# Performance work log

Hardware: AMD Instinct MI355X
Metric: run time of the kernel (lower is better)

## Reference

```python
import jax, jax.numpy as jnp
import numpy as np

N_NODES = 50000
N_EDGES = 800000
N_GRAPHS = 64
IN_CH = 128
HID_G = 256
HID_FC = 256
OUT_CH = 128


def setup_inputs() -> dict:
    key = jax.random.key(0)
    ks = jax.random.split(key, 16)
    x = jax.random.normal(ks[0], (N_NODES, IN_CH), dtype=jnp.float32)
    edge_index = jax.random.randint(ks[1], (2, N_EDGES), 0, N_NODES, dtype=jnp.int64)
    batch = jnp.sort(jax.random.randint(ks[2], (N_NODES,), 0, N_GRAPHS, dtype=jnp.int64))
    hlr = jax.random.normal(ks[3], (N_GRAPHS, 1), dtype=jnp.float32)
    std = jax.random.normal(ks[4], (N_GRAPHS, 1), dtype=jnp.float32)
    s = 0.05
    W0 = jax.random.normal(ks[5], (IN_CH, HID_G), dtype=jnp.float32) * s
    b0 = jnp.zeros((HID_G,), jnp.float32)
    W1 = jax.random.normal(ks[6], (HID_G, HID_G), dtype=jnp.float32) * s
    b1 = jnp.zeros((HID_G,), jnp.float32)
    W2 = jax.random.normal(ks[7], (HID_G, HID_G), dtype=jnp.float32) * s
    b2 = jnp.zeros((HID_G,), jnp.float32)
    fcW0 = jax.random.normal(ks[8], (HID_G + 2, HID_FC), dtype=jnp.float32) * s
    fcb0 = jnp.zeros((HID_FC,), jnp.float32)
    fcW1 = jax.random.normal(ks[9], (HID_FC, OUT_CH), dtype=jnp.float32) * s
    fcb1 = jnp.zeros((OUT_CH,), jnp.float32)
    return dict(x=x, edge_index=edge_index, batch=batch, hlr=hlr, std=std,
                W0=W0, b0=b0, W1=W1, b1=b1, W2=W2, b2=b2,
                fcW0=fcW0, fcb0=fcb0, fcW1=fcW1, fcb1=fcb1)


def _gcn_conv(h, W, b, src, dst, dis):
    # GCNConv with added self-loops and symmetric normalization:
    # out_i = sum_{j->i} d_j^{-1/2} d_i^{-1/2} (h_j W) + d_i^{-1} (h_i W) + b
    hW = h @ W  # [N, F]
    norm = dis[src] * dis[dst]  # [E]
    agg = jax.ops.segment_sum(hW[src] * norm[:, None], dst, num_segments=N_NODES)
    agg = agg + hW * (dis * dis)[:, None]  # self-loop contribution
    return agg + b


def reference(x, edge_index, batch, hlr, std, W0, b0, W1, b1, W2, b2, fcW0, fcb0, fcW1, fcb1):
    src, dst = edge_index[0], edge_index[1]
    # degree on A + I (edge weight 1), computed at destination nodes
    deg = jax.ops.segment_sum(jnp.ones((N_EDGES,), x.dtype), dst, num_segments=N_NODES) + 1.0
    dis = jax.lax.rsqrt(deg)
    h = jax.nn.relu(_gcn_conv(x, W0, b0, src, dst, dis))
    h = jax.nn.relu(_gcn_conv(h, W1, b1, src, dst, dis))
    h = jax.nn.relu(_gcn_conv(h, W2, b2, src, dst, dis))
    # global mean pool over graphs
    counts = jax.ops.segment_sum(jnp.ones((N_NODES,), x.dtype), batch, num_segments=N_GRAPHS)
    pooled = jax.ops.segment_sum(h, batch, num_segments=N_GRAPHS) / jnp.maximum(counts, 1.0)[:, None]
    z = jnp.concatenate([pooled, hlr, std], axis=1)  # [G, HID_G + 2]
    z = jax.nn.relu(z @ fcW0 + fcb0)
    return z @ fcW1 + fcb1
```

## Files before the change

kernel.cpp:

```cpp
#include <hip/hip_runtime.h>

#define NNODES 50000
#define NEDGES 800000
#define NGRAPHS 64
#define INCH 128
#define HID 256
#define ZSTR (HID + 2)
#define SCAN_B 512
#define SCAN_NB ((NNODES + SCAN_B - 1) / SCAN_B)
#define NSLICE 16

typedef __attribute__((ext_vector_type(8))) short short8v;
typedef __attribute__((ext_vector_type(8))) unsigned short ushort8v;
typedef __attribute__((ext_vector_type(4))) float f32x4;

__device__ inline ushort f2b(float f) {
    union { float f; unsigned u; } v; v.f = f;
    unsigned r = (v.u + 0x7FFFu + ((v.u >> 16) & 1u)) >> 16;
    return (ushort)r;
}
__device__ inline float b2f(ushort b) {
    union { unsigned u; float f; } v; v.u = ((unsigned)b) << 16;
    return v.f;
}

__global__ __launch_bounds__(256) void fill_pre(const int* __restrict__ dst, int* __restrict__ deg,
                                                unsigned char* __restrict__ pwn) {
    int e = blockIdx.x * 256 + threadIdx.x;
    if (e < NEDGES) pwn[e] = (unsigned char)atomicAdd(&deg[dst[e]], 1);
}

__global__ __launch_bounds__(256) void dis_kernel(const int* __restrict__ deg, float* __restrict__ dis) {
    int i = blockIdx.x * 256 + threadIdx.x;
    if (i < NNODES) dis[i] = rsqrtf((float)deg[i] + 1.0f);
}

__global__ __launch_bounds__(SCAN_B) void scan1(const int* __restrict__ deg, int* __restrict__ row_ptr,
                                                int* __restrict__ bsum) {
    __shared__ int s[SCAN_B];
    int t = threadIdx.x;
    int i = blockIdx.x * SCAN_B + t;
    int v = (i < NNODES) ? deg[i] : 0;
    s[t] = v;
    __syncthreads();
    for (int off = 1; off < SCAN_B; off <<= 1) {
        int x = (t >= off) ? s[t - off] : 0;
        __syncthreads();
        if (t >= off) s[t] += x;
        __syncthreads();
    }
    if (i < NNODES) row_ptr[i + 1] = s[t];
    if (t == SCAN_B - 1) bsum[blockIdx.x] = s[t];
}

__global__ __launch_bounds__(128) void scan2(int* __restrict__ bsum) {
    __shared__ int s[128];
    int t = threadIdx.x;
    int v = (t < SCAN_NB) ? bsum[t] : 0;
    s[t] = v;
    __syncthreads();
    for (int off = 1; off < 128; off <<= 1) {
        int x = (t >= off) ? s[t - off] : 0;
        __syncthreads();
        if (t >= off) s[t] += x;
        __syncthreads();
    }
    if (t < SCAN_NB) bsum[t] = s[t];
}

__global__ __launch_bounds__(SCAN_B) void scan3(int* __restrict__ row_ptr, const int* __restrict__ bsum) {
    int b = blockIdx.x, t = threadIdx.x;
    int i = b * SCAN_B + t;
    if (i == 0) row_ptr[0] = 0;
    if (i < NNODES && b > 0) row_ptr[i + 1] += bsum[b - 1];
}

__global__ __launch_bounds__(256) void fill_scatter(const int* __restrict__ src, const int* __restrict__ dst,
                                                    const unsigned char* __restrict__ pwn,
                                                    const int* __restrict__ row_ptr,
                                                    ushort* __restrict__ csr_src) {
    int e = blockIdx.x * 256 + threadIdx.x;
    if (e >= NEDGES) return;
    int d = dst[e];
    csr_src[row_ptr[d] + pwn[e]] = (ushort)src[e];
}

__global__ __launch_bounds__(256) void xcvt(const float4* __restrict__ x, const float* __restrict__ dis,
                                            ushort4* __restrict__ xb, int n4) {
    int i = blockIdx.x * 256 + threadIdx.x;
    if (i >= n4) return;
    float d = dis[i >> 5];
    float4 v = x[i];
    ushort4 o;
    o.x = f2b(d * v.x); o.y = f2b(d * v.y); o.z = f2b(d * v.z); o.w = f2b(d * v.w);
    xb[i] = o;
}

__global__ __launch_bounds__(256) void wcvt(const float* __restrict__ W, ushort* __restrict__ Wt, int K, int N) {
    int i = blockIdx.x * 256 + threadIdx.x;
    if (i >= K * N) return;
    int k = i / N, n = i - k * N;
    Wt[n * K + k] = f2b(W[i]);
}

template <int K>
__global__ __launch_bounds__(512, 4) void gcn_fused(const ushort* __restrict__ hin,
                                                    const int* __restrict__ row_ptr,
                                                    const ushort* __restrict__ csr_src,
                                                    const ushort* __restrict__ Bt,
                                                    const float* __restrict__ bias,
                                                    const float* __restrict__ dis,
                                                    ushort* __restrict__ hout, int scale_out) {
    __shared__ ushort As[128 * K];
    const int tid = threadIdx.x;
    const int w = tid >> 6, l = tid & 63;
    const int R0 = blockIdx.x * 128;

    constexpr int CHL = K / 8;
    constexpr int NPW = 64 / CHL;
    const int sub = l / CHL;
    const int lane = l - sub * CHL;
    const ushort* hp = hin + lane * 8;
#pragma unroll
    for (int it = 0; it < 128 / (8 * NPW); ++it) {
        int nloc = (it * 8 + w) * NPW + sub;
        int node = R0 + nloc;
        ushort8v o;
        if (node < NNODES) {
            ushort8v sv = *(const ushort8v*)&hp[(size_t)node * K];
            float a0 = b2f(sv[0]), a1 = b2f(sv[1]), a2 = b2f(sv[2]), a3 = b2f(sv[3]);
            float a4 = b2f(sv[4]), a5 = b2f(sv[5]), a6 = b2f(sv[6]), a7 = b2f(sv[7]);
            int e = row_ptr[node], e1 = row_ptr[node + 1];
            for (; e + 7 < e1; e += 8) {
                ushort8v v[8];
#pragma unroll
                for (int u = 0; u < 8; ++u) v[u] = *(const ushort8v*)&hp[(size_t)csr_src[e + u] * K];
#pragma unroll
                for (int u = 0; u < 8; ++u) {
                    a0 += b2f(v[u][0]); a1 += b2f(v[u][1]); a2 += b2f(v[u][2]); a3 += b2f(v[u][3]);
                    a4 += b2f(v[u][4]); a5 += b2f(v[u][5]); a6 += b2f(v[u][6]); a7 += b2f(v[u][7]);
                }
            }
            for (; e < e1; ++e) {
                ushort8v v0 = *(const ushort8v*)&hp[(size_t)csr_src[e] * K];
                a0 += b2f(v0[0]); a1 += b2f(v0[1]); a2 += b2f(v0[2]); a3 += b2f(v0[3]);
                a4 += b2f(v0[4]); a5 += b2f(v0[5]); a6 += b2f(v0[6]); a7 += b2f(v0[7]);
            }
            o[0] = f2b(a0); o[1] = f2b(a1); o[2] = f2b(a2); o[3] = f2b(a3);
            o[4] = f2b(a4); o[5] = f2b(a5); o[6] = f2b(a6); o[7] = f2b(a7);
        } else {
            o = ushort8v{0, 0, 0, 0, 0, 0, 0, 0};
        }
        *(ushort8v*)&As[nloc * K + ((lane * 8) ^ ((nloc & 7) * 8))] = o;
    }
    __syncthreads();

    const int wr = w >> 2, wc = w & 3;
    const int r16 = l & 15, kg = l >> 4;
    f32x4 acc[4][4] = {};
#pragma unroll
    for (int k0 = 0; k0 < K; k0 += 32) {
        int k = k0 + kg * 8;
        short8v a[4], b[4];
#pragma unroll
        for (int m = 0; m < 4; ++m) {
            int row = wr * 64 + m * 16 + r16;
            a[m] = *(const short8v*)&As[row * K + (k ^ ((row & 7) * 8))];
        }
#pragma unroll
        for (int n = 0; n < 4; ++n)
            b[n] = *(const short8v*)&Bt[(size_t)(wc * 64 + n * 16 + r16) * K + k];
#pragma unroll
        for (int m = 0; m < 4; ++m)
#pragma unroll
            for (int n = 0; n < 4; ++n)
                acc[m][n] = __builtin_amdgcn_mfma_f32_16x16x32_bf16(a[m], b[n], acc[m][n], 0, 0, 0);
    }
    float bv[4];
#pragma unroll
    for (int n = 0; n < 4; ++n) bv[n] = bias[wc * 64 + n * 16 + r16];
#pragma unroll
    for (int m = 0; m < 4; ++m) {
#pragma unroll
        for (int j = 0; j < 4; ++j) {
            int row = R0 + wr * 64 + m * 16 + kg * 4 + j;
            if (row >= NNODES) continue;
            float dr = dis[row];
            float os = scale_out ? dr : 1.0f;
#pragma unroll
            for (int n = 0; n < 4; ++n) {
                float v = fmaxf(dr * acc[m][n][j] + bv[n], 0.f) * os;
                hout[(size_t)row * HID + wc * 64 + n * 16 + r16] = f2b(v);
            }
        }
    }
}

__global__ __launch_bounds__(256) void graph_bounds(const int* __restrict__ batch, int* __restrict__ gstart) {
    int i = blockIdx.x * 256 + threadIdx.x;
    if (i >= NNODES) return;
    int b = batch[i];
    if (i == 0) {
        for (int g = 0; g <= b; ++g) gstart[g] = 0;
    } else {
        int pb = batch[i - 1];
        for (int g = pb + 1; g <= b; ++g) gstart[g] = i;
    }
    if (i == NNODES - 1) {
        for (int g = b + 1; g <= NGRAPHS; ++g) gstart[g] = NNODES;
    }
}

__global__ __launch_bounds__(HID) void pool_partial(const ushort* __restrict__ h, const int* __restrict__ gstart,
                                                    float* __restrict__ z) {
    int g = blockIdx.x;
    int s = blockIdx.y;
    int t = threadIdx.x;
    int n0 = gstart[g], n1 = gstart[g + 1];
    int cnt = n1 - n0;
    if (cnt <= 0) return;
    int len = (cnt + NSLICE - 1) / NSLICE;
    int a = n0 + s * len;
    int b = a + len < n1 ? a + len : n1;
    if (a >= b) return;
    float acc = 0.f;
    for (int n = a; n < b; ++n) acc += b2f(h[(size_t)n * HID + t]);
    atomicAdd(&z[g * ZSTR + t], acc);
}

__global__ __launch_bounds__(HID) void pool_finalize(const int* __restrict__ gstart, const float* __restrict__ hlr,
                                                     const float* __restrict__ stdv, float* __restrict__ z) {
    int g = blockIdx.x;
    int t = threadIdx.x;
    int cnt = gstart[g + 1] - gstart[g];
    float inv = 1.f / (float)(cnt > 0 ? cnt : 1);
    z[g * ZSTR + t] *= inv;
    if (t == 0) {
        z[g * ZSTR + HID] = hlr[g];
        z[g * ZSTR + HID + 1] = stdv[g];
    }
}

__global__ __launch_bounds__(HID) void fc_k(const float* __restrict__ z, const float* __restrict__ fcW0,
                                            const float* __restrict__ fcb0, const float* __restrict__ fcW1,
                                            const float* __restrict__ fcb1, float* __restrict__ out) {
    __shared__ float zs[ZSTR];
    __shared__ float z2[HID];
    int g = blockIdx.x;
    int t = threadIdx.x;
    zs[t] = z[g * ZSTR + t];
    if (t < 2) zs[HID + t] = z[g * ZSTR + HID + t];
    __syncthreads();
    float acc = fcb0[t];
    for (int k = 0; k < ZSTR; ++k) acc += zs[k] * fcW0[k * HID + t];
    z2[t] = fmaxf(acc, 0.f);
    __syncthreads();
    if (t < INCH) {
        float acc2 = fcb1[t];
        for (int k = 0; k < HID; ++k) acc2 += z2[k] * fcW1[k * INCH + t];
        out[g * INCH + t] = acc2;
    }
}

extern "C" void kernel_launch(void* const* d_in, const int* in_sizes, int n_in,
                              void* d_out, int out_size, void* d_ws, size_t ws_size,
                              hipStream_t stream) {
    const float* x = (const float*)d_in[0];
    const int* ei = (const int*)d_in[1];
    const int* src = ei;
    const int* dst = ei + NEDGES;
    const int* batch = (const int*)d_in[2];
    const float* hlr = (const float*)d_in[3];
    const float* stdv = (const float*)d_in[4];
    const float* W0 = (const float*)d_in[5];
    const float* b0 = (const float*)d_in[6];
    const float* W1 = (const float*)d_in[7];
    const float* b1 = (const float*)d_in[8];
    const float* W2 = (const float*)d_in[9];
    const float* b2 = (const float*)d_in[10];
    const float* fcW0 = (const float*)d_in[11];
    const float* fcb0 = (const float*)d_in[12];
    const float* fcW1 = (const float*)d_in[13];
    const float* fcb1 = (const float*)d_in[14];
    float* out = (float*)d_out;

    char* p = (char*)d_ws;
    auto alloc = [&](size_t bytes) -> char* {
        char* r = p;
        p += (bytes + 255) & ~(size_t)255;
        return r;
    };
    ushort* xb = (ushort*)alloc(sizeof(ushort) * (size_t)NNODES * INCH);
    ushort* h = (ushort*)alloc(sizeof(ushort) * (size_t)NNODES * HID);
    ushort* hb = (ushort*)alloc(sizeof(ushort) * (size_t)NNODES * HID);
    ushort* Wt0 = (ushort*)alloc(sizeof(ushort) * HID * INCH);
    ushort* Wt1 = (ushort*)alloc(sizeof(ushort) * HID * HID);
    ushort* Wt2 = (ushort*)alloc(sizeof(ushort) * HID * HID);
    float* dis = (float*)alloc(sizeof(float) * NNODES);
    int* deg = (int*)alloc(sizeof(int) * NNODES);
    int* row_ptr = (int*)alloc(sizeof(int) * (NNODES + 1));
    unsigned char* pwn = (unsigned char*)alloc(sizeof(unsigned char) * NEDGES);
    ushort* csr_src = (ushort*)alloc(sizeof(ushort) * NEDGES);
    int* bsum = (int*)alloc(sizeof(int) * 128);
    int* gstart = (int*)alloc(sizeof(int) * (NGRAPHS + 1));
    float* z = (float*)alloc(sizeof(float) * NGRAPHS * ZSTR);
    (void)ws_size; (void)in_sizes; (void)n_in; (void)out_size;

    const int eblocks = (NEDGES + 255) / 256;

    hipMemsetAsync(deg, 0, sizeof(int) * NNODES, stream);
    fill_pre<<<eblocks, 256, 0, stream>>>(dst, deg, pwn);
    dis_kernel<<<(NNODES + 255) / 256, 256, 0, stream>>>(deg, dis);
    scan1<<<SCAN_NB, SCAN_B, 0, stream>>>(deg, row_ptr, bsum);
    scan2<<<1, 128, 0, stream>>>(bsum);
    scan3<<<SCAN_NB, SCAN_B, 0, stream>>>(row_ptr, bsum);
    fill_scatter<<<eblocks, 256, 0, stream>>>(src, dst, pwn, row_ptr, csr_src);

    xcvt<<<(NNODES * INCH / 4 + 255) / 256, 256, 0, stream>>>((const float4*)x, dis, (ushort4*)xb,
                                                              NNODES * INCH / 4);
    wcvt<<<(INCH * HID + 255) / 256, 256, 0, stream>>>(W0, Wt0, INCH, HID);
    wcvt<<<(HID * HID + 255) / 256, 256, 0, stream>>>(W1, Wt1, HID, HID);
    wcvt<<<(HID * HID + 255) / 256, 256, 0, stream>>>(W2, Wt2, HID, HID);

    const int gblocks = (NNODES + 127) / 128;
    gcn_fused<INCH><<<gblocks, 512, 0, stream>>>(xb, row_ptr, csr_src, Wt0, b0, dis, h, 1);
    gcn_fused<HID><<<gblocks, 512, 0, stream>>>(h, row_ptr, csr_src, Wt1, b1, dis, hb, 1);
    gcn_fused<HID><<<gblocks, 512, 0, stream>>>(hb, row_ptr, csr_src, Wt2, b2, dis, h, 0);

    graph_bounds<<<(NNODES + 255) / 256, 256, 0, stream>>>(batch, gstart);
    hipMemsetAsync(z, 0, sizeof(float) * NGRAPHS * ZSTR, stream);
    dim3 pgrid(NGRAPHS, NSLICE);
    pool_partial<<<pgrid, HID, 0, stream>>>(h, gstart, z);
    pool_finalize<<<NGRAPHS, HID, 0, stream>>>(gstart, hlr, stdv, z);
    fc_k<<<NGRAPHS, HID, 0, stream>>>(z, fcW0, fcb0, fcW1, fcb1, out);
}
```

Baseline: 330.9 us.

## Fuse global mean-pool accumulation into the last GCN layer epilogue

The third GCN layer no longer writes its bf16 output to global memory. Instead it accumulates per-graph column sums in registers and shared memory (two graph slots per 128-row block), then atomically adds them into z. This removes the 25 MB store and reread of h and the separate pool_partial launch. In exchange it adds shared-memory and global atomics, plus a direct global-atomic path for blocks that span more than two graphs. Pooling now sums fp32 values instead of bf16-rounded ones.

```diff
diff --git a/kernel.cpp b/kernel.cpp
--- a/kernel.cpp
+++ b/kernel.cpp
@@ -8,7 +8,6 @@
 #define ZSTR (HID + 2)
 #define SCAN_B 512
 #define SCAN_NB ((NNODES + SCAN_B - 1) / SCAN_B)
-#define NSLICE 16
 
 typedef __attribute__((ext_vector_type(8))) short short8v;
 typedef __attribute__((ext_vector_type(8))) unsigned short ushort8v;
@@ -103,18 +102,24 @@
     Wt[n * K + k] = f2b(W[i]);
 }
 
-template <int K>
+template <int K, bool POOL>
 __global__ __launch_bounds__(512, 4) void gcn_fused(const ushort* __restrict__ hin,
                                                     const int* __restrict__ row_ptr,
                                                     const ushort* __restrict__ csr_src,
                                                     const ushort* __restrict__ Bt,
                                                     const float* __restrict__ bias,
                                                     const float* __restrict__ dis,
-                                                    ushort* __restrict__ hout, int scale_out) {
+                                                    ushort* __restrict__ hout, int scale_out,
+                                                    const int* __restrict__ batch, float* __restrict__ z) {
     __shared__ ushort As[128 * K];
+    __shared__ float z_loc[2][HID];
     const int tid = threadIdx.x;
     const int w = tid >> 6, l = tid & 63;
     const int R0 = blockIdx.x * 128;
+
+    if (POOL) {
+        z_loc[tid >> 8][tid & 255] = 0.f;
+    }
 
     constexpr int CHL = K / 8;
     constexpr int NPW = 64 / CHL;
@@ -179,19 +184,59 @@
     float bv[4];
 #pragma unroll
     for (int n = 0; n < 4; ++n) bv[n] = bias[wc * 64 + n * 16 + r16];
-#pragma unroll
-    for (int m = 0; m < 4; ++m) {
-#pragma unroll
-        for (int j = 0; j < 4; ++j) {
-            int row = R0 + wr * 64 + m * 16 + kg * 4 + j;
-            if (row >= NNODES) continue;
-            float dr = dis[row];
-            float os = scale_out ? dr : 1.0f;
-#pragma unroll
-            for (int n = 0; n < 4; ++n) {
-                float v = fmaxf(dr * acc[m][n][j] + bv[n], 0.f) * os;
-                hout[(size_t)row * HID + wc * 64 + n * 16 + r16] = f2b(v);
+
+    if (!POOL) {
+#pragma unroll
+        for (int m = 0; m < 4; ++m) {
+#pragma unroll
+            for (int j = 0; j < 4; ++j) {
+                int row = R0 + wr * 64 + m * 16 + kg * 4 + j;
+                if (row >= NNODES) continue;
+                float dr = dis[row];
+                float os = scale_out ? dr : 1.0f;
+#pragma unroll
+                for (int n = 0; n < 4; ++n) {
+                    float v = fmaxf(dr * acc[m][n][j] + bv[n], 0.f) * os;
+                    hout[(size_t)row * HID + wc * 64 + n * 16 + r16] = f2b(v);
+                }
             }
+        }
+    } else {
+        const int g0 = batch[R0];
+        float psum[2][4] = {{0.f, 0.f, 0.f, 0.f}, {0.f, 0.f, 0.f, 0.f}};
+#pragma unroll
+        for (int m = 0; m < 4; ++m) {
+#pragma unroll
+            for (int j = 0; j < 4; ++j) {
+                int row = R0 + wr * 64 + m * 16 + kg * 4 + j;
+                if (row >= NNODES) continue;
+                float dr = dis[row];
+                int slot = batch[row] - g0;
+#pragma unroll
+                for (int n = 0; n < 4; ++n) {
+                    float v = fmaxf(dr * acc[m][n][j] + bv[n], 0.f);
+                    if (slot <= 1) {
+                        psum[slot][n] += v;
+                    } else {
+                        atomicAdd(&z[(size_t)(g0 + slot) * ZSTR + wc * 64 + n * 16 + r16], v);
+                    }
+                }
+            }
+        }
+#pragma unroll
+        for (int s = 0; s < 2; ++s)
+#pragma unroll
+            for (int n = 0; n < 4; ++n)
+                if (psum[s][n] != 0.f) atomicAdd(&z_loc[s][wc * 64 + n * 16 + r16], psum[s][n]);
+        __syncthreads();
+        int last = R0 + 127;
+        if (last > NNODES - 1) last = NNODES - 1;
+        const int g_last = batch[last];
+        const int s = tid >> 8;
+        const int ch = tid & 255;
+        if (g0 + s <= g_last && g0 + s < NGRAPHS) {
+            float v = z_loc[s][ch];
+            if (v != 0.f) atomicAdd(&z[(size_t)(g0 + s) * ZSTR + ch], v);
         }
     }
 }
@@ -209,23 +254,6 @@
     if (i == NNODES - 1) {
         for (int g = b + 1; g <= NGRAPHS; ++g) gstart[g] = NNODES;
     }
-}
-
-__global__ __launch_bounds__(HID) void pool_partial(const ushort* __restrict__ h, const int* __restrict__ gstart,
-                                                    float* __restrict__ z) {
-    int g = blockIdx.x;
-    int s = blockIdx.y;
-    int t = threadIdx.x;
-    int n0 = gstart[g], n1 = gstart[g + 1];
-    int cnt = n1 - n0;
-    if (cnt <= 0) return;
-    int len = (cnt + NSLICE - 1) / NSLICE;
-    int a = n0 + s * len;
-    int b = a + len < n1 ? a + len : n1;
-    if (a >= b) return;
-    float acc = 0.f;
-    for (int n = a; n < b; ++n) acc += b2f(h[(size_t)n * HID + t]);
-    atomicAdd(&z[g * ZSTR + t], acc);
 }
 
 __global__ __launch_bounds__(HID) void pool_finalize(const int* __restrict__ gstart, const float* __restrict__ hlr,
@@ -309,6 +337,7 @@
     const int eblocks = (NEDGES + 255) / 256;
 
     hipMemsetAsync(deg, 0, sizeof(int) * NNODES, stream);
+    hipMemsetAsync(z, 0, sizeof(float) * NGRAPHS * ZSTR, stream);
     fill_pre<<<eblocks, 256, 0, stream>>>(dst, deg, pwn);
     dis_kernel<<<(NNODES + 255) / 256, 256, 0, stream>>>(deg, dis);
     scan1<<<SCAN_NB, SCAN_B, 0, stream>>>(deg, row_ptr, bsum);
@@ -323,14 +352,11 @@
     wcvt<<<(HID * HID + 255) / 256, 256, 0, stream>>>(W2, Wt2, HID, HID);
 
     const int gblocks = (NNODES + 127) / 128;
-    gcn_fused<INCH><<<gblocks, 512, 0, stream>>>(xb, row_ptr, csr_src, Wt0, b0, dis, h, 1);
-    gcn_fused<HID><<<gblocks, 512, 0, stream>>>(h, row_ptr, csr_src, Wt1, b1, dis, hb, 1);
-    gcn_fused<HID><<<gblocks, 512, 0, stream>>>(hb, row_ptr, csr_src, Wt2, b2, dis, h, 0);
+    gcn_fused<INCH, false><<<gblocks, 512, 0, stream>>>(xb, row_ptr, csr_src, Wt0, b0, dis, h, 1, batch, z);
+    gcn_fused<HID, false><<<gblocks, 512, 0, stream>>>(h, row_ptr, csr_src, Wt1, b1, dis, hb, 1, batch, z);
+    gcn_fused<HID, true><<<gblocks, 512, 0, stream>>>(hb, row_ptr, csr_src, Wt2, b2, dis, h, 0, batch, z);
 
     graph_bounds<<<(NNODES + 255) / 256, 256, 0, stream>>>(batch, gstart);
-    hipMemsetAsync(z, 0, sizeof(float) * NGRAPHS * ZSTR, stream);
-    dim3 pgrid(NGRAPHS, NSLICE);
-    pool_partial<<<pgrid, HID, 0, stream>>>(h, gstart, z);
     pool_finalize<<<NGRAPHS, HID, 0, stream>>>(gstart, hlr, stdv, z);
     fc_k<<<NGRAPHS, HID, 0, stream>>>(z, fcW0, fcb0, fcW1, fcb1, out);
 }
```

Result: faster. 319.9 us, median of 2 (-3.3%).
